# Performance work log

Measured on AMD Instinct MI355X. Metric: run time of the kernel, lower is better.

The kernel has to match this reference:

```python
import jax, jax.numpy as jnp
import numpy as np

N, CIN, COUT = 16, 64, 64
HIN, WIN = 66, 66
KH, KW = 3, 3
HOUT, WOUT = HIN - KH + 1, WIN - KW + 1  # 64, 64 (stride=1, pad=0, dil=1)


def setup_inputs() -> dict:
    key = jax.random.key(0)
    k1, k2, k3 = jax.random.split(key, 3)
    inp = jax.random.normal(k1, (N, CIN, HIN, WIN), dtype=jnp.float32)
    offset = jax.random.normal(k2, (N, 2 * KH * KW, HOUT, WOUT), dtype=jnp.float32)
    weight = jax.random.normal(k3, (COUT, CIN, KH, KW), dtype=jnp.float32) * 0.05
    return {"input": inp, "offset": offset, "weight": weight}


def _deform_conv2d(inp, offset, weight):
    # torchvision.ops.deform_conv2d with stride=1, pad=0, dilation=1,
    # offset_groups=1, no modulation mask, no bias.
    n, c, h, w = inp.shape
    cout, cin, kh, kw = weight.shape
    k = kh * kw
    _, _, ho, wo = offset.shape
    dt = inp.dtype

    # offset layout: channel 2*k is dy, 2*k+1 is dx for kernel tap k
    off = offset.reshape(n, k, 2, ho, wo)
    kh_idx = (jnp.arange(k) // kw).astype(dt)  # [K]
    kw_idx = (jnp.arange(k) % kw).astype(dt)
    base_y = jnp.arange(ho, dtype=dt)[None, :, None] + kh_idx[:, None, None]  # [K,Ho,1]
    base_x = jnp.arange(wo, dtype=dt)[None, None, :] + kw_idx[:, None, None]  # [K,1,Wo]
    py = base_y[None] + off[:, :, 0]  # [N,K,Ho,Wo] sampling y coords
    px = base_x[None] + off[:, :, 1]  # [N,K,Ho,Wo] sampling x coords

    y0 = jnp.floor(py)
    x0 = jnp.floor(px)
    fy = py - y0  # bilinear fractions
    fx = px - x0
    y0i = y0.astype(jnp.int32)
    x0i = x0.astype(jnp.int32)

    def gather(yi, xi):
        # zero padding outside the image: mask out-of-bounds corners
        valid = ((yi >= 0) & (yi < h) & (xi >= 0) & (xi < w)).astype(dt)
        yc = jnp.clip(yi, 0, h - 1)
        xc = jnp.clip(xi, 0, w - 1)
        # per-batch fancy gather: [N,C,K,Ho,Wo]
        g = jax.vmap(lambda xn, yn, xn2: xn[:, yn, xn2])(inp, yc, xc)
        return g * valid[:, None]

    val = (gather(y0i, x0i) * ((1 - fy) * (1 - fx))[:, None]
           + gather(y0i, x0i + 1) * ((1 - fy) * fx)[:, None]
           + gather(y0i + 1, x0i) * (fy * (1 - fx))[:, None]
           + gather(y0i + 1, x0i + 1) * (fy * fx)[:, None])  # [N,C,K,Ho,Wo]

    wk = weight.reshape(cout, cin, k)
    return jnp.einsum('nckhw,ock->nohw', val, wk)


def reference(input, offset, weight):
    return _deform_conv2d(input, offset, weight)
```

## Files before the change

kernel.cpp:

```cpp
#include <hip/hip_runtime.h>
#include <hip/hip_bf16.h>

#define NB    16
#define CIN   64
#define COUT  64
#define HIN   66
#define WIN   66
#define HOUT  64
#define WOUT  64
#define KK    9
#define NXCD  8

typedef __attribute__((ext_vector_type(8))) short bf16x8;
typedef __attribute__((ext_vector_type(4))) float f32x4;
typedef __attribute__((ext_vector_type(2))) float f32x2;

static __device__ __forceinline__ unsigned int pkbf(float lo, float hi) {
    union { __hip_bfloat162 b; unsigned int u; } x;
    x.b = __float22bfloat162_rn(make_float2(lo, hi));
    return x.u;
}

static __device__ __forceinline__ f32x2 up2(unsigned int w) {
    f32x2 r;
    r.x = __uint_as_float(w << 16);
    r.y = __uint_as_float(w & 0xFFFF0000u);
    return r;
}

static __device__ __forceinline__ unsigned int blend_word(unsigned int d00, unsigned int d01,
                                                          unsigned int d10, unsigned int d11,
                                                          f32x2 W00, f32x2 W01, f32x2 W10, f32x2 W11) {
    f32x2 v = W00 * up2(d00);
    v += W01 * up2(d01);
    v += W10 * up2(d10);
    v += W11 * up2(d11);
    return pkbf(v.x, v.y);
}

__global__ __launch_bounds__(256) void repack_all(const float* __restrict__ in,
                                                  const float* __restrict__ w,
                                                  unsigned short* __restrict__ nhwc,
                                                  unsigned short* __restrict__ wF) {
    int b = blockIdx.x;
    if (b < NB * HIN) {
        int n = b / HIN, y = b % HIN;
        __shared__ float buf[CIN * 67];
        const float* src = in + (size_t)(n * CIN) * HIN * WIN + y * WIN;
        for (int i = threadIdx.x; i < CIN * WIN; i += 256) {
            int c = i / WIN, x = i - c * WIN;
            buf[c * 67 + x] = src[c * (HIN * WIN) + x];
        }
        __syncthreads();
        unsigned int* dst = (unsigned int*)(nhwc + (size_t)((n * HIN + y) * WIN) * CIN);
        for (int i = threadIdx.x; i < WIN * (CIN / 2); i += 256) {
            int x = i >> 5, c2 = (i & 31) * 2;
            dst[x * 32 + (c2 >> 1)] = pkbf(buf[c2 * 67 + x], buf[(c2 + 1) * 67 + x]);
        }
    } else {
        int i = (b - NB * HIN) * 256 + threadIdx.x;
        if (i >= 4 * 18 * 64 * 8) return;
        int j    = i & 7;
        int t    = i >> 3;
        int lane = t & 63;  t >>= 6;
        int ksg  = t % 18;
        int ct   = t / 18;
        int kb = ksg / 6, ks = ksg % 6;
        int klocal = ks * 32 + (lane >> 4) * 8 + j;
        int tap = kb * 3 + (klocal >> 6);
        int cin = klocal & 63;
        int cout = ct * 16 + (lane & 15);
        wF[i] = (unsigned short)(pkbf(w[(cout * CIN + cin) * KK + tap], 0.f) & 0xFFFF);
    }
}

struct GB { int4 u0, u1, u2, u3; int2 aw; int p; };

__global__ __launch_bounds__(256, 4) void dconv8(const unsigned short* __restrict__ nhwc,
                                                 const float* __restrict__ off,
                                                 const unsigned short* __restrict__ wF,
                                                 float* __restrict__ out) {
    __shared__ __align__(16) char sm[31488];
    char* smS = sm;
    int*  sAv = (int*)(sm + 24576);
    int2* sAw = (int2*)(sm + 26880);

    const int tid  = threadIdx.x;
    const int lane = tid & 63;
    const int wv   = tid >> 6;
    const int p0 = blockIdx.x;
    const int logical = (p0 & (NXCD - 1)) * (NB * HOUT / NXCD) + (p0 >> 3);
    const int n  = logical >> 6;
    const int ho = logical & 63;

    const unsigned short* nh = nhwc + (size_t)n * (HIN * WIN * CIN);
    const float* off_n = off + (size_t)n * (2 * KK * HOUT * WOUT) + ho * WOUT;

    for (int q = tid; q < KK * 64; q += 256) {
        int k  = q >> 6;
        int wo = q & 63;
        float dy = off_n[(2 * k) * (HOUT * WOUT) + wo];
        float dx = off_n[(2 * k + 1) * (HOUT * WOUT) + wo];
        int kh = (k * 171) >> 9;
        int kw = k - 3 * kh;
        float py = (float)(ho + kh) + dy;
        float px = (float)(wo + kw) + dx;
        float y0f = floorf(py), x0f = floorf(px);
        float fy = py - y0f, fx = px - x0f;
        int y0 = (int)y0f, x0 = (int)x0f;
        int y1 = y0 + 1,   x1 = x0 + 1;
        float vy0 = (y0 >= 0 && y0 < HIN) ? 1.f : 0.f;
        float vy1 = (y1 >= 0 && y1 < HIN) ? 1.f : 0.f;
        float vx0 = (x0 >= 0 && x0 < WIN) ? 1.f : 0.f;
        float vx1 = (x1 >= 0 && x1 < WIN) ? 1.f : 0.f;
        int y0c = min(max(y0, 0), HIN - 1), y1c = min(max(y1, 0), HIN - 1);
        int x0c = min(max(x0, 0), WIN - 1), x1c = min(max(x1, 0), WIN - 1);
        int a00 = (y0c * WIN + x0c) * CIN;
        int sx  = x1c - x0c;
        int sy  = y1c - y0c;
        sAv[q] = a00 | (sx << 20) | (sy << 21);
        float ax0 = vx0 * (1.f - fx), ax1 = vx1 * fx;
        float ay0 = vy0 * (1.f - fy), ay1 = vy1 * fy;
        sAw[q] = make_int2((int)pkbf(ax0, ax1), (int)pkbf(ay0, ay1));
    }
    __syncthreads();

    f32x4 acc[4];
#pragma unroll
    for (int rt = 0; rt < 4; ++rt) acc[rt] = (f32x4){0.f, 0.f, 0.f, 0.f};

    const int c0  = (lane & 7) * 8;
    const int grp = lane >> 3;
    const int h   = lane >> 4;

#define LOADP(G, KB, J) do {                                           \
        int p_ = wv * 48 + ((J) >> 1) * 16 + ((J) & 1) * 8 + grp;      \
        int q_ = (KB) * 192 + p_;                                      \
        int av_ = sAv[q_];                                             \
        G.aw = sAw[q_];                                                \
        int a_  = (av_ & 0xFFFFF) + c0;                                \
        int dx_ = (av_ >> 14) & 64;                                    \
        int dy_ = ((av_ >> 21) & 1) * (WIN * CIN);                     \
        G.u0 = *(const int4*)(nh + a_);                                \
        G.u1 = *(const int4*)(nh + a_ + dx_);                          \
        G.u2 = *(const int4*)(nh + a_ + dy_);                          \
        G.u3 = *(const int4*)(nh + a_ + dy_ + dx_);                    \
        G.p = p_;                                                      \
    } while (0)

#define PROCP(G) do {                                                  \
        f32x2 AX = up2((unsigned int)G.aw.x);                          \
        f32x2 AY = up2((unsigned int)G.aw.y);                          \
        f32x2 W00 = {AY.x * AX.x, AY.x * AX.x};                        \
        f32x2 W01 = {AY.x * AX.y, AY.x * AX.y};                        \
        f32x2 W10 = {AY.y * AX.x, AY.y * AX.x};                        \
        f32x2 W11 = {AY.y * AX.y, AY.y * AX.y};                        \
        int4 r_;                                                       \
        r_.x = (int)blend_word(G.u0.x, G.u1.x, G.u2.x, G.u3.x, W00, W01, W10, W11); \
        r_.y = (int)blend_word(G.u0.y, G.u1.y, G.u2.y, G.u3.y, W00, W01, W10, W11); \
        r_.z = (int)blend_word(G.u0.z, G.u1.z, G.u2.z, G.u3.z, W00, W01, W10, W11); \
        r_.w = (int)blend_word(G.u0.w, G.u1.w, G.u2.w, G.u3.w, W00, W01, W10, W11); \
        int k3_ = G.p >> 6, wo_ = G.p & 63;                            \
        int sl_ = (k3_ * 8 + (lane & 7)) ^ (wo_ & 7);                  \
        *(int4*)(smS + wo_ * 384 + (sl_ << 4)) = r_;                   \
    } while (0)

    GB a0, a1;
    LOADP(a0, 0, 0);

#pragma unroll
    for (int kb = 0; kb < 3; ++kb) {
        bf16x8 breg[6];
#pragma unroll
        for (int ks = 0; ks < 6; ++ks)
            breg[ks] = *(const bf16x8*)(wF + (((wv * 18 + kb * 6 + ks) << 6) + lane) * 8);

        LOADP(a1, kb, 1); PROCP(a0);
        LOADP(a0, kb, 2); PROCP(a1);
        LOADP(a1, kb, 3); PROCP(a0);
        LOADP(a0, kb, 4); PROCP(a1);
        LOADP(a1, kb, 5); PROCP(a0);
        PROCP(a1);
        __syncthreads();

        if (kb < 2) LOADP(a0, kb + 1, 0);

#pragma unroll
        for (int rt = 0; rt < 4; ++rt) {
            const int row = rt * 16 + (lane & 15);
#pragma unroll
            for (int ks = 0; ks < 6; ++ks) {
                int aslot = (ks * 4 + h) ^ (row & 7);
                bf16x8 af = *(const bf16x8*)(smS + row * 384 + (aslot << 4));
                acc[rt] = __builtin_amdgcn_mfma_f32_16x16x32_bf16(af, breg[ks], acc[rt], 0, 0, 0);
            }
        }
        __syncthreads();
    }
#undef LOADP
#undef PROCP

    float* red = (float*)sm;
#pragma unroll
    for (int rt = 0; rt < 4; ++rt)
#pragma unroll
        for (int r = 0; r < 4; ++r)
            red[(16 * wv + (lane & 15)) * 65 + (16 * rt + h * 4 + r)] = acc[rt][r];
    __syncthreads();
    float* op = out + (size_t)(n * COUT) * (HOUT * WOUT) + ho * WOUT + lane;
#pragma unroll
    for (int j = 0; j < 16; ++j) {
        int co = wv * 16 + j;
        op[(size_t)co * (HOUT * WOUT)] = red[co * 65 + lane];
    }
}

__global__ __launch_bounds__(256) void repack_w_kernel(const float* __restrict__ w,
                                                       float* __restrict__ wT) {
    int i = blockIdx.x * 256 + threadIdx.x;
    if (i >= KK * CIN * COUT) return;
    int co = i & 63; int t = i >> 6;
    int c = t & 63;  int k = t >> 6;
    wT[i] = w[(co * CIN + c) * KK + k];
}

__global__ __launch_bounds__(256) void dconv_kernel(const float* __restrict__ inp,
                                                    const float* __restrict__ off,
                                                    const float* __restrict__ wT,
                                                    float* __restrict__ out) {
    const int tid = threadIdx.x;
    const int wo  = tid & 63;
    const int g   = tid >> 6;
    const int p   = blockIdx.x;
    const int logical = (p & (NXCD - 1)) * (NB * HOUT / NXCD) + (p >> 3);
    const int n   = logical >> 6;
    const int ho  = logical & 63;
    const int cbase = __builtin_amdgcn_readfirstlane(g << 4);
    float acc[COUT];
#pragma unroll
    for (int i = 0; i < COUT; ++i) acc[i] = 0.f;
    const float* inp_n = inp + n * (CIN * HIN * WIN);
    const float* off_p = off + ((n * (2 * KK)) * HOUT + ho) * WOUT + wo;
#pragma unroll 1
    for (int k = 0; k < KK; ++k) {
        float dy = off_p[(2 * k) * (HOUT * WOUT)];
        float dx = off_p[(2 * k + 1) * (HOUT * WOUT)];
        float py = (float)(ho + k / 3) + dy;
        float px = (float)(wo + k % 3) + dx;
        float y0f = floorf(py), x0f = floorf(px);
        float fy = py - y0f, fx = px - x0f;
        int y0 = (int)y0f, x0 = (int)x0f;
        int y1 = y0 + 1,   x1 = x0 + 1;
        float vy0 = (y0 >= 0 && y0 < HIN) ? 1.f : 0.f;
        float vy1 = (y1 >= 0 && y1 < HIN) ? 1.f : 0.f;
        float vx0 = (x0 >= 0 && x0 < WIN) ? 1.f : 0.f;
        float vx1 = (x1 >= 0 && x1 < WIN) ? 1.f : 0.f;
        int y0c = min(max(y0, 0), HIN - 1), y1c = min(max(y1, 0), HIN - 1);
        int x0c = min(max(x0, 0), WIN - 1), x1c = min(max(x1, 0), WIN - 1);
        int o00 = y0c * WIN + x0c, o01 = y0c * WIN + x1c;
        int o10 = y1c * WIN + x0c, o11 = y1c * WIN + x1c;
        float w00 = (1.f - fy) * (1.f - fx) * vy0 * vx0;
        float w01 = (1.f - fy) * fx * vy0 * vx1;
        float w10 = fy * (1.f - fx) * vy1 * vx0;
        float w11 = fy * fx * vy1 * vx1;
        const float* pc   = inp_n + cbase * (HIN * WIN);
        const float* wrow = wT + ((k * CIN + cbase) << 6);
#pragma unroll 4
        for (int c = 0; c < 16; ++c) {
            float v = w00 * pc[o00] + w01 * pc[o01] + w10 * pc[o10] + w11 * pc[o11];
#pragma unroll
            for (int co = 0; co < COUT; ++co) acc[co] = fmaf(v, wrow[co], acc[co]);
            pc += HIN * WIN; wrow += COUT;
        }
    }
    __shared__ float redf[COUT * WOUT];
    for (int i = tid; i < COUT * WOUT; i += 256) redf[i] = 0.f;
    __syncthreads();
#pragma unroll
    for (int co = 0; co < COUT; ++co) atomicAdd(&redf[co * WOUT + wo], acc[co]);
    __syncthreads();
    float* out_p = out + (n * COUT * HOUT + ho) * WOUT;
    for (int i = tid; i < COUT * WOUT; i += 256) {
        int co = i >> 6, w2 = i & 63;
        out_p[co * (HOUT * WOUT) + w2] = redf[i];
    }
}

extern "C" void kernel_launch(void* const* d_in, const int* in_sizes, int n_in,
                              void* d_out, int out_size, void* d_ws, size_t ws_size,
                              hipStream_t stream) {
    const float* inp = (const float*)d_in[0];
    const float* off = (const float*)d_in[1];
    const float* w   = (const float*)d_in[2];
    float* out = (float*)d_out;

    const size_t nhwc_bytes = (size_t)NB * HIN * WIN * CIN * 2;
    const size_t wF_bytes   = (size_t)4 * 18 * 64 * 8 * 2;

    if (ws_size >= nhwc_bytes + wF_bytes) {
        unsigned short* nhwc = (unsigned short*)d_ws;
        unsigned short* wF   = (unsigned short*)((char*)d_ws + nhwc_bytes);
        repack_all<<<NB * HIN + 144, 256, 0, stream>>>(inp, w, nhwc, wF);
        dconv8<<<NB * HOUT, 256, 0, stream>>>(nhwc, off, wF, out);
    } else {
        float* wT = (float*)d_ws;
        repack_w_kernel<<<(KK * CIN * COUT + 255) / 256, 256, 0, stream>>>(w, wT);
        dconv_kernel<<<NB * HOUT, 256, 0, stream>>>(inp, off, wT, out);
    }
}
```

Baseline: 34.40 us.

## Deepen gather prefetch to three buffers and widen repack stores

The deformable-conv kernel now keeps three gather buffers in flight instead of two, issuing two bilinear-corner loads ahead of each blend. The blend weights are read from shared memory at blend time rather than held in registers, which frees registers for the extra buffer. The repack kernel remaps blocks across XCDs and writes four channels per 64-bit store instead of two per 32-bit store. The deeper prefetch aims to hide global gather latency but raises register pressure under the 4-waves launch bound, with a risk of spills.

New measurement: 31.06 us (median of 2 runs). 1.11x faster.

```diff
diff --git a/kernel.cpp b/kernel.cpp
--- a/kernel.cpp
+++ b/kernel.cpp
@@ -44,7 +44,8 @@
                                                   unsigned short* __restrict__ wF) {
     int b = blockIdx.x;
     if (b < NB * HIN) {
-        int n = b / HIN, y = b % HIN;
+        int l = (b & 7) * (NB * HIN / 8) + (b >> 3);
+        int n = l / HIN, y = l % HIN;
         __shared__ float buf[CIN * 67];
         const float* src = in + (size_t)(n * CIN) * HIN * WIN + y * WIN;
         for (int i = threadIdx.x; i < CIN * WIN; i += 256) {
@@ -52,10 +53,12 @@
             buf[c * 67 + x] = src[c * (HIN * WIN) + x];
         }
         __syncthreads();
-        unsigned int* dst = (unsigned int*)(nhwc + (size_t)((n * HIN + y) * WIN) * CIN);
-        for (int i = threadIdx.x; i < WIN * (CIN / 2); i += 256) {
-            int x = i >> 5, c2 = (i & 31) * 2;
-            dst[x * 32 + (c2 >> 1)] = pkbf(buf[c2 * 67 + x], buf[(c2 + 1) * 67 + x]);
+        int2* dst = (int2*)(nhwc + (size_t)((n * HIN + y) * WIN) * CIN);
+        for (int i = threadIdx.x; i < WIN * (CIN / 4); i += 256) {
+            int x = i >> 4, c4 = (i & 15) * 4;
+            dst[x * 16 + (c4 >> 2)] =
+                make_int2((int)pkbf(buf[c4 * 67 + x], buf[(c4 + 1) * 67 + x]),
+                          (int)pkbf(buf[(c4 + 2) * 67 + x], buf[(c4 + 3) * 67 + x]));
         }
     } else {
         int i = (b - NB * HIN) * 256 + threadIdx.x;
@@ -74,9 +77,9 @@
     }
 }
 
-struct GB { int4 u0, u1, u2, u3; int2 aw; int p; };
-
-__global__ __launch_bounds__(256, 4) void dconv8(const unsigned short* __restrict__ nhwc,
+struct GB { int4 u0, u1, u2, u3; int q; };
+
+__global__ __launch_bounds__(256, 4) void dconv9(const unsigned short* __restrict__ nhwc,
                                                  const float* __restrict__ off,
                                                  const unsigned short* __restrict__ wF,
                                                  float* __restrict__ out) {
@@ -134,10 +137,8 @@
     const int h   = lane >> 4;
 
 #define LOADP(G, KB, J) do {                                           \
-        int p_ = wv * 48 + ((J) >> 1) * 16 + ((J) & 1) * 8 + grp;      \
-        int q_ = (KB) * 192 + p_;                                      \
+        int q_ = (KB) * 192 + wv * 48 + ((J) >> 1) * 16 + ((J) & 1) * 8 + grp; \
         int av_ = sAv[q_];                                             \
-        G.aw = sAw[q_];                                                \
         int a_  = (av_ & 0xFFFFF) + c0;                                \
         int dx_ = (av_ >> 14) & 64;                                    \
         int dy_ = ((av_ >> 21) & 1) * (WIN * CIN);                     \
@@ -145,12 +146,13 @@
         G.u1 = *(const int4*)(nh + a_ + dx_);                          \
         G.u2 = *(const int4*)(nh + a_ + dy_);                          \
         G.u3 = *(const int4*)(nh + a_ + dy_ + dx_);                    \
-        G.p = p_;                                                      \
+        G.q = q_;                                                      \
     } while (0)
 
 #define PROCP(G) do {                                                  \
-        f32x2 AX = up2((unsigned int)G.aw.x);                          \
-        f32x2 AY = up2((unsigned int)G.aw.y);                          \
+        int2 aw_ = sAw[G.q];                                           \
+        f32x2 AX = up2((unsigned int)aw_.x);                           \
+        f32x2 AY = up2((unsigned int)aw_.y);                           \
         f32x2 W00 = {AY.x * AX.x, AY.x * AX.x};                        \
         f32x2 W01 = {AY.x * AX.y, AY.x * AX.y};                        \
         f32x2 W10 = {AY.y * AX.x, AY.y * AX.x};                        \
@@ -160,13 +162,15 @@
         r_.y = (int)blend_word(G.u0.y, G.u1.y, G.u2.y, G.u3.y, W00, W01, W10, W11); \
         r_.z = (int)blend_word(G.u0.z, G.u1.z, G.u2.z, G.u3.z, W00, W01, W10, W11); \
         r_.w = (int)blend_word(G.u0.w, G.u1.w, G.u2.w, G.u3.w, W00, W01, W10, W11); \
-        int k3_ = G.p >> 6, wo_ = G.p & 63;                            \
+        int wo_ = G.q & 63;                                            \
+        int k3_ = (G.q >> 6) % 3;                                      \
         int sl_ = (k3_ * 8 + (lane & 7)) ^ (wo_ & 7);                  \
         *(int4*)(smS + wo_ * 384 + (sl_ << 4)) = r_;                   \
     } while (0)
 
-    GB a0, a1;
+    GB a0, a1, a2;
     LOADP(a0, 0, 0);
+    LOADP(a1, 0, 1);
 
 #pragma unroll
     for (int kb = 0; kb < 3; ++kb) {
@@ -175,15 +179,18 @@
         for (int ks = 0; ks < 6; ++ks)
             breg[ks] = *(const bf16x8*)(wF + (((wv * 18 + kb * 6 + ks) << 6) + lane) * 8);
 
-        LOADP(a1, kb, 1); PROCP(a0);
-        LOADP(a0, kb, 2); PROCP(a1);
-        LOADP(a1, kb, 3); PROCP(a0);
-        LOADP(a0, kb, 4); PROCP(a1);
-        LOADP(a1, kb, 5); PROCP(a0);
+        LOADP(a2, kb, 2); PROCP(a0);
+        LOADP(a0, kb, 3); PROCP(a1);
+        LOADP(a1, kb, 4); PROCP(a2);
+        LOADP(a2, kb, 5); PROCP(a0);
         PROCP(a1);
+        PROCP(a2);
         __syncthreads();
 
-        if (kb < 2) LOADP(a0, kb + 1, 0);
+        if (kb < 2) {
+            LOADP(a0, kb + 1, 0);
+            LOADP(a1, kb + 1, 1);
+        }
 
 #pragma unroll
         for (int rt = 0; rt < 4; ++rt) {
@@ -301,7 +308,7 @@
         unsigned short* nhwc = (unsigned short*)d_ws;
         unsigned short* wF   = (unsigned short*)((char*)d_ws + nhwc_bytes);
         repack_all<<<NB * HIN + 144, 256, 0, stream>>>(inp, w, nhwc, wF);
-        dconv8<<<NB * HOUT, 256, 0, stream>>>(nhwc, off, wF, out);
+        dconv9<<<NB * HOUT, 256, 0, stream>>>(nhwc, off, wF, out);
     } else {
         float* wT = (float*)d_ws;
         repack_w_kernel<<<(KK * CIN * COUT + 255) / 256, 256, 0, stream>>>(w, wT);
```
